# Kernel tuning notes

Hardware: AMD Instinct MI355X
Metric: run time of the kernel (lower is better)

The kernel has to match this reference:

```python
import jax, jax.numpy as jnp
import numpy as np

EMBED_DIM = 1024
NUM_HEADS = 16
HEAD_DIM = EMBED_DIM // NUM_HEADS
SEQ_LEN = 2048
BATCH = 2
THETA_BASE = 10000.0


def rope_angles(head_dim, max_seq_len):
    inv_freq = 1.0 / (THETA_BASE ** (jnp.arange(0, head_dim, 2, dtype=jnp.float32) / head_dim))
    pos = jnp.arange(max_seq_len, dtype=jnp.float32)
    angles = pos[:, None] * inv_freq[None, :]              # [S, D/2]
    angles = jnp.concatenate([angles, angles], axis=-1)    # [S, D]
    return jnp.cos(angles), jnp.sin(angles)


def apply_rope(x, cos, sin):
    # x: [B, H, S, D]; cos/sin: [S, D]
    d = x.shape[-1]
    x1, x2 = x[..., : d // 2], x[..., d // 2 :]
    rotated = jnp.concatenate([-x2, x1], axis=-1)
    return x * cos[None, None, :, :] + rotated * sin[None, None, :, :]


def setup_inputs() -> dict:
    key = jax.random.key(0)
    kx, kq, kk, kv, ko = jax.random.split(key, 5)
    s = 1.0 / np.sqrt(EMBED_DIM)
    return {
        "x": jax.random.normal(kx, (BATCH, SEQ_LEN, EMBED_DIM), dtype=jnp.float32),
        "Wq": jax.random.normal(kq, (EMBED_DIM, EMBED_DIM), dtype=jnp.float32) * s,
        "Wk": jax.random.normal(kk, (EMBED_DIM, EMBED_DIM), dtype=jnp.float32) * s,
        "Wv": jax.random.normal(kv, (EMBED_DIM, EMBED_DIM), dtype=jnp.float32) * s,
        "Wo": jax.random.normal(ko, (EMBED_DIM, EMBED_DIM), dtype=jnp.float32) * s,
    }


def reference(x, Wq, Wk, Wv, Wo):
    B, S, E = x.shape
    H, D = NUM_HEADS, HEAD_DIM
    cos, sin = rope_angles(D, S)

    def split_heads(t):
        return t.reshape(B, S, H, D).transpose(0, 2, 1, 3)  # [B,H,S,D]

    q = split_heads(x @ Wq.T)
    k = split_heads(x @ Wk.T)
    v = split_heads(x @ Wv.T)

    q = apply_rope(q, cos, sin)
    k = apply_rope(k, cos, sin)

    scores = jnp.einsum("bhsd,bhtd->bhst", q, k)
    causal = jnp.triu(jnp.ones((S, S), dtype=bool), k=1)
    scores = jnp.where(causal[None, None, :, :], -jnp.inf, scores)
    weights = jax.nn.softmax(scores / jnp.sqrt(jnp.float32(D)), axis=-1)

    ctx = jnp.einsum("bhst,bhtd->bhsd", weights, v)
    ctx = ctx.transpose(0, 2, 1, 3).reshape(B, S, E)
    return ctx @ Wo.T
```

## Files before the change

### kernel.cpp

```cpp
#include <hip/hip_runtime.h>
#include <hip/hip_bf16.h>

#define H_NUM 16
#define D_DIM 64
#define S_LEN 2048
#define EMB   1024
#define M_TOT 4096

typedef unsigned short u16;
typedef unsigned int   u32;
typedef __attribute__((ext_vector_type(8))) short short8;
typedef __attribute__((ext_vector_type(4))) float f32x4;

__device__ __forceinline__ u32 f2bf_u(float f) {
    u32 u = __float_as_uint(f);
    return (u + 0x7fffu + ((u >> 16) & 1u)) >> 16;
}
__device__ __forceinline__ u32 pack2(float a, float b) {
    return f2bf_u(a) | (f2bf_u(b) << 16);
}
__device__ __forceinline__ u32 pack2t(float a, float b) {
    return __builtin_amdgcn_perm(__float_as_uint(b), __float_as_uint(a),
                                 0x07060302u);
}
__device__ __forceinline__ uint4 pack8(float4 lo, float4 hi) {
    return make_uint4(pack2(lo.x, lo.y), pack2(lo.z, lo.w),
                      pack2(hi.x, hi.y), pack2(hi.z, hi.w));
}

__device__ __forceinline__ void lds_dma16(const u16* g, u16* l) {
    __builtin_amdgcn_global_load_lds(
        (const __attribute__((address_space(1))) void*)g,
        (__attribute__((address_space(3))) void*)l, 16, 0, 0);
}

__global__ __launch_bounds__(256) void cast_kernel(
    const float* __restrict__ x,  const float* __restrict__ Wq,
    const float* __restrict__ Wk, const float* __restrict__ Wv,
    const float* __restrict__ Wo, u16* __restrict__ ws, float2* __restrict__ tab)
{
    const int seg = blockIdx.y;
    if (seg == 5) {
        const int idx = blockIdx.x * 256 + threadIdx.x;
        if (idx < S_LEN * 32) {
            const int s = idx >> 5, d = idx & 31;
            const float ang = (float)s * __expf(-(float)d * 0.28782313662425573f);
            tab[idx] = make_float2(cosf(ang), sinf(ang));
        }
        return;
    }
    const float* src = (seg == 0) ? x : (seg == 1) ? Wq : (seg == 2) ? Wk
                     : (seg == 3) ? Wv : Wo;
    u16* dst = (seg == 0) ? ws : ws + (3 + seg) * 1048576;
    const int n = (seg == 0) ? 4194304 : 1048576;
    const int idx = (blockIdx.x * 256 + threadIdx.x) * 8;
    if (idx < n) {
        float4 lo = *(const float4*)(src + idx);
        float4 hi = *(const float4*)(src + idx + 4);
        *(uint4*)(dst + idx) = pack8(lo, hi);
    }
}

__global__ __launch_bounds__(256) void qkv_rope_kernel(
    const u16* __restrict__ xb, const u16* __restrict__ wb,
    const float2* __restrict__ tab,
    u16* __restrict__ qo, u16* __restrict__ ko, u16* __restrict__ vo)
{
    const int w  = blockIdx.y >> 3;
    const int nb = blockIdx.y & 7;
    const u16* W = wb + w * 1048576;

    __shared__ __align__(16) u16 smem[12288];
    u16* As = smem;
    u16* Bs = smem + 64 * 64;
    u16 (*Ep)[132] = (u16(*)[132])smem;

    const int tid   = threadIdx.x;
    const int lane  = tid & 63;
    const int wid   = tid >> 6;
    const int waveM = wid >> 1;
    const int waveN = wid & 1;
    const int col16 = lane & 15;
    const int quad  = lane >> 4;

    const int m0 = blockIdx.x * 64;
    const int n0 = nb * 128;

    f32x4 acc[2][4];
    const f32x4 zero4 = {0.f, 0.f, 0.f, 0.f};
#pragma unroll
    for (int i = 0; i < 2; i++)
#pragma unroll
        for (int j = 0; j < 4; j++) acc[i][j] = zero4;

    const int drow = tid >> 3;
    const int dpos = tid & 7;
    const u16* Ag = xb + (size_t)m0 * EMB;
    const u16* Bg = W  + (size_t)n0 * EMB;

    for (int k0 = 0; k0 < EMB; k0 += 64) {
        __syncthreads();
#pragma unroll
        for (int j = 0; j < 2; j++) {
            const int rl = j * 32 + drow;
            const int cg = dpos ^ (rl & 7);
            lds_dma16(Ag + (size_t)rl * EMB + k0 + cg * 8,
                      As + (j * 32 + wid * 8) * 64);
        }
#pragma unroll
        for (int j = 0; j < 4; j++) {
            const int rl = j * 32 + drow;
            const int cg = dpos ^ (rl & 7);
            lds_dma16(Bg + (size_t)rl * EMB + k0 + cg * 8,
                      Bs + (j * 32 + wid * 8) * 64);
        }
        __syncthreads();

        short8 af[2][2], bf[4][2];
#pragma unroll
        for (int mt = 0; mt < 2; mt++) {
            const int r = waveM * 32 + mt * 16 + col16;
#pragma unroll
            for (int ks = 0; ks < 2; ks++) {
                const int p = (ks * 4 + quad) ^ (r & 7);
                af[mt][ks] = *(const short8*)(As + r * 64 + p * 8);
            }
        }
#pragma unroll
        for (int nt = 0; nt < 4; nt++) {
            const int r = waveN * 64 + nt * 16 + col16;
#pragma unroll
            for (int ks = 0; ks < 2; ks++) {
                const int p = (ks * 4 + quad) ^ (r & 7);
                bf[nt][ks] = *(const short8*)(Bs + r * 64 + p * 8);
            }
        }
#pragma unroll
        for (int ks = 0; ks < 2; ks++)
#pragma unroll
            for (int mt = 0; mt < 2; mt++)
#pragma unroll
                for (int nt = 0; nt < 4; nt++)
                    acc[mt][nt] = __builtin_amdgcn_mfma_f32_16x16x32_bf16(
                        af[mt][ks], bf[nt][ks], acc[mt][nt], 0, 0, 0);
    }

    const float qs = (w == 0) ? 0.18033688011112042f : 1.0f;
    __syncthreads();
#pragma unroll
    for (int mt = 0; mt < 2; mt++) {
#pragma unroll
        for (int r = 0; r < 4; r++) {
            const int m_local = waveM * 32 + mt * 16 + quad * 4 + r;
            const int s = (m0 + m_local) & 2047;
            if (w == 2) {
#pragma unroll
                for (int nt = 0; nt < 4; nt++)
                    Ep[m_local][waveN * 64 + nt * 16 + col16] =
                        (u16)f2bf_u(acc[mt][nt][r]);
            } else {
#pragma unroll
                for (int nt = 0; nt < 2; nt++) {
                    const int d = nt * 16 + col16;
                    const float2 cs = tab[s * 32 + d];
                    const float lo = acc[mt][nt][r];
                    const float hi = acc[mt][nt + 2][r];
                    Ep[m_local][waveN * 64 + d]      =
                        (u16)f2bf_u((lo * cs.x - hi * cs.y) * qs);
                    Ep[m_local][waveN * 64 + d + 32] =
                        (u16)f2bf_u((hi * cs.x + lo * cs.y) * qs);
                }
            }
        }
    }
    __syncthreads();

    const int b = m0 >> 11;
    if (w != 2) {
        u16* out = (w == 0) ? qo : ko;
#pragma unroll
        for (int j = 0; j < 4; j++) {
            const int g = j * 256 + tid;
            const int head_local = g >> 9;
            const int sl  = (g >> 3) & 63;
            const int cir = g & 7;
            uint4 val = *(const uint4*)(&Ep[sl][head_local * 64 + cir * 8]);
            const int h = (n0 >> 6) + head_local;
            const size_t base = (((size_t)(b * H_NUM + h)) * S_LEN + (m0 & 2047)) * 64;
            *(uint4*)(out + base + (size_t)(g & 511) * 8) = val;
        }
    } else {
        const int s0 = m0 & 2047;
#pragma unroll
        for (int j = 0; j < 4; j++) {
            const int g = j * 256 + tid;
            const int d_all = g >> 3;
            const int sc = g & 7;
            u32 wv[4];
#pragma unroll
            for (int hw = 0; hw < 4; hw++) {
                const int p0 = sc * 8 + hw * 2;
                const int r0 = ((p0 & 3) << 4) | (p0 >> 2);
                const int p1 = p0 + 1;
                const int r1 = ((p1 & 3) << 4) | (p1 >> 2);
                wv[hw] = (u32)Ep[r0][d_all] | ((u32)Ep[r1][d_all] << 16);
            }
            const int h = (n0 >> 6) + (d_all >> 6);
            const int d = d_all & 63;
            *(uint4*)(vo + ((size_t)(b * H_NUM + h) * 64 + d) * 2048 + s0 + sc * 8) =
                make_uint4(wv[0], wv[1], wv[2], wv[3]);
        }
    }
}

__global__ __launch_bounds__(256) void attn_kernel(
    const u16* __restrict__ q, const u16* __restrict__ k,
    const u16* __restrict__ v, u16* __restrict__ ctx)
{
    __shared__ __align__(16) u16 QPA[64 * 64];
    __shared__ __align__(16) u16 QPB[64 * 64];
    __shared__ __align__(16) u16 Ks[2][64 * 64];
    __shared__ __align__(16) u16 VTs[2][64 * 64];

    const int tid   = threadIdx.x;
    const int lane  = tid & 63;
    const int wid   = tid >> 6;
    const int col16 = lane & 15;
    const int quad  = lane >> 4;

    const int bh = blockIdx.x;
    const int p  = blockIdx.y;
    const int qbA = p;
    const int qbB = 31 - p;
    const int qBaseA = qbA * 64;
    const int qBaseB = qbB * 64;
    const size_t bhOff = (size_t)bh * S_LEN * D_DIM;

    const int drow = tid >> 3;
    const int dpos = tid & 7;

    auto stage = [&](int kt, int buf) {
#pragma unroll
        for (int j = 0; j < 2; j++) {
            const int rl = j * 32 + drow;
            const int cg = dpos ^ (rl & 7);
            lds_dma16(k + bhOff + (size_t)(kt * 64 + rl) * 64 + cg * 8,
                      &Ks[buf][(j * 32 + wid * 8) * 64]);
        }
#pragma unroll
        for (int j = 0; j < 2; j++) {
            const int rl = j * 32 + drow;
            const int cg = dpos ^ (rl & 7);
            lds_dma16(v + bhOff + (size_t)rl * 2048 + kt * 64 + cg * 8,
                      &VTs[buf][(j * 32 + wid * 8) * 64]);
        }
    };

    stage(0, 0);
#pragma unroll
    for (int j = 0; j < 2; j++) {
        const int rl = j * 32 + drow;
        const int cg = dpos ^ (rl & 7);
        lds_dma16(q + bhOff + (size_t)(qBaseA + rl) * 64 + cg * 8,
                  QPA + (j * 32 + wid * 8) * 64);
        lds_dma16(q + bhOff + (size_t)(qBaseB + rl) * 64 + cg * 8,
                  QPB + (j * 32 + wid * 8) * 64);
    }
    __syncthreads();

    short8 qfA[2], qfB[2];
    {
        const int rq = wid * 16 + col16;
#pragma unroll
        for (int ks = 0; ks < 2; ks++) {
            const int c = (ks * 4 + quad) ^ (rq & 7);
            qfA[ks] = *(const short8*)(QPA + rq * 64 + c * 8);
            qfB[ks] = *(const short8*)(QPB + rq * 64 + c * 8);
        }
    }

    const short ONE = (short)0x3F80;
    const short8 onesf = {ONE, ONE, ONE, ONE, ONE, ONE, ONE, ONE};

    f32x4 OA[4], OB[4];
    const f32x4 zero4 = {0.f, 0.f, 0.f, 0.f};
#pragma unroll
    for (int j = 0; j < 4; j++) { OA[j] = zero4; OB[j] = zero4; }
    f32x4 laccA = zero4, laccB = zero4;

    auto process = [&](const short8* qf, u16* QP, f32x4* O, f32x4& lacc,
                       int qBase, bool diag, int kt, int cur) {
        f32x4 sc[4];
#pragma unroll
        for (int nt = 0; nt < 4; nt++) sc[nt] = zero4;
#pragma unroll
        for (int ks = 0; ks < 2; ks++) {
            short8 kf[4];
#pragma unroll
            for (int nt = 0; nt < 4; nt++) {
                const int rk = nt * 16 + col16;
                const int c = (ks * 4 + quad) ^ (rk & 7);
                kf[nt] = *(const short8*)(&Ks[cur][rk * 64 + c * 8]);
            }
            __builtin_amdgcn_s_setprio(1);
#pragma unroll
            for (int nt = 0; nt < 4; nt++)
                sc[nt] = __builtin_amdgcn_mfma_f32_16x16x32_bf16(
                    qf[ks], kf[nt], sc[nt], 0, 0, 0);
            __builtin_amdgcn_s_setprio(0);
        }

        if (diag) {
#pragma unroll
            for (int r = 0; r < 4; r++) {
                const int qg = qBase + wid * 16 + quad * 4 + r;
#pragma unroll
                for (int nt = 0; nt < 4; nt++) {
                    const int kg = kt * 64 + nt * 16 + col16;
                    float pv = __builtin_amdgcn_exp2f(sc[nt][r]);
                    if (kg > qg) pv = 0.f;
                    sc[nt][r] = pv;
                }
            }
        } else {
#pragma unroll
            for (int r = 0; r < 4; r++) {
#pragma unroll
                for (int nt = 0; nt < 4; nt++)
                    sc[nt][r] = __builtin_amdgcn_exp2f(sc[nt][r]);
            }
        }

#pragma unroll
        for (int r = 0; r < 4; r++) {
            const int ml = quad * 4 + r;
            const u32 lo = pack2t(sc[0][r], sc[1][r]);
            const u32 hi = pack2t(sc[2][r], sc[3][r]);
            *(uint2*)(QP + (wid * 16 + ml) * 64 +
                      (((col16 >> 1) ^ (ml & 7)) * 8 + (col16 & 1) * 4)) =
                make_uint2(lo, hi);
        }

#pragma unroll
        for (int ks = 0; ks < 2; ks++) {
            short8 pf, vf[4];
            {
                const int c = (ks * 4 + quad) ^ (col16 & 7);
                pf = *(const short8*)(QP + (wid * 16 + col16) * 64 + c * 8);
            }
#pragma unroll
            for (int dt = 0; dt < 4; dt++) {
                const int d = dt * 16 + col16;
                const int c = (ks * 4 + quad) ^ (d & 7);
                vf[dt] = *(const short8*)(&VTs[cur][d * 64 + c * 8]);
            }
            __builtin_amdgcn_s_setprio(1);
#pragma unroll
            for (int dt = 0; dt < 4; dt++)
                O[dt] = __builtin_amdgcn_mfma_f32_16x16x32_bf16(
                    pf, vf[dt], O[dt], 0, 0, 0);
            lacc = __builtin_amdgcn_mfma_f32_16x16x32_bf16(
                pf, onesf, lacc, 0, 0, 0);
            __builtin_amdgcn_s_setprio(0);
        }
    };

    for (int kt = 0; kt <= qbB; kt++) {
        if (kt > 0) __syncthreads();
        if (kt < qbB) stage(kt + 1, (kt + 1) & 1);
        const int cur = kt & 1;

        process(qfB, QPB, OB, laccB, qBaseB, kt == qbB, kt, cur);
        if (kt <= qbA)
            process(qfA, QPA, OA, laccA, qBaseA, kt == qbA, kt, cur);
    }

    const int b = bh >> 4, h = bh & 15;
    auto epilogue = [&](u16* QP, f32x4* O, f32x4& lacc, int qBase) {
#pragma unroll
        for (int r = 0; r < 4; r++) {
            const int ml = quad * 4 + r;
            const float inv = __builtin_amdgcn_rcpf(lacc[r]);
            const u32 lo = pack2t(O[0][r] * inv, O[1][r] * inv);
            const u32 hi = pack2t(O[2][r] * inv, O[3][r] * inv);
            *(uint2*)(QP + (wid * 16 + ml) * 64 +
                      (((col16 >> 1) ^ (ml & 7)) * 8 + (col16 & 1) * 4)) =
                make_uint2(lo, hi);
        }
#pragma unroll
        for (int j = 0; j < 2; j++) {
            const int gg  = j * 64 + lane;
            const int sl = gg >> 3;
            const int cir = gg & 7;
            u32 wv[4];
#pragma unroll
            for (int hw = 0; hw < 4; hw++) {
                const int d0 = cir * 8 + hw * 2;
                const int p0 = ((d0 & 15) << 2) | (d0 >> 4);
                const int d1 = d0 + 1;
                const int p1 = ((d1 & 15) << 2) | (d1 >> 4);
                const u16 v0 = QP[(wid * 16 + sl) * 64 + ((p0 >> 3) ^ (sl & 7)) * 8 + (p0 & 7)];
                const u16 v1 = QP[(wid * 16 + sl) * 64 + ((p1 >> 3) ^ (sl & 7)) * 8 + (p1 & 7)];
                wv[hw] = (u32)v0 | ((u32)v1 << 16);
            }
            const size_t rowbase =
                ((size_t)b * S_LEN + qBase + wid * 16 + sl) * EMB + h * 64;
            *(uint4*)(ctx + rowbase + cir * 8) = make_uint4(wv[0], wv[1], wv[2], wv[3]);
        }
    };
    epilogue(QPA, OA, laccA, qBaseA);
    epilogue(QPB, OB, laccB, qBaseB);
}

__global__ __launch_bounds__(256) void proj_kernel(
    const u16* __restrict__ X, const u16* __restrict__ W, float* __restrict__ out)
{
    __shared__ __align__(16) u16 smem[8192];
    u16* As = smem;
    u16* Bs = smem + 64 * 64;

    const int tid   = threadIdx.x;
    const int lane  = tid & 63;
    const int wid   = tid >> 6;
    const int col16 = lane & 15;
    const int quad  = lane >> 4;

    const int m0 = blockIdx.x * 64;
    const int n0 = blockIdx.y * 64;

    f32x4 acc[4];
    const f32x4 zero4 = {0.f, 0.f, 0.f, 0.f};
#pragma unroll
    for (int i = 0; i < 4; i++) acc[i] = zero4;

    const int drow = tid >> 3;
    const int dpos = tid & 7;
    const u16* Ag = X + (size_t)m0 * EMB;
    const u16* Bg = W + (size_t)n0 * EMB;

    for (int k0 = 0; k0 < EMB; k0 += 64) {
        __syncthreads();
#pragma unroll
        for (int j = 0; j < 2; j++) {
            const int rl = j * 32 + drow;
            const int cg = dpos ^ (rl & 7);
            lds_dma16(Ag + (size_t)rl * EMB + k0 + cg * 8,
                      As + (j * 32 + wid * 8) * 64);
        }
#pragma unroll
        for (int j = 0; j < 2; j++) {
            const int rl = j * 32 + drow;
            const int cg = dpos ^ (rl & 7);
            lds_dma16(Bg + (size_t)rl * EMB + k0 + cg * 8,
                      Bs + (j * 32 + wid * 8) * 64);
        }
        __syncthreads();

        short8 af[2], bf[4][2];
        {
            const int r = wid * 16 + col16;
#pragma unroll
            for (int ks = 0; ks < 2; ks++) {
                const int p = (ks * 4 + quad) ^ (r & 7);
                af[ks] = *(const short8*)(As + r * 64 + p * 8);
            }
        }
#pragma unroll
        for (int nt = 0; nt < 4; nt++) {
            const int r = nt * 16 + col16;
#pragma unroll
            for (int ks = 0; ks < 2; ks++) {
                const int p = (ks * 4 + quad) ^ (r & 7);
                bf[nt][ks] = *(const short8*)(Bs + r * 64 + p * 8);
            }
        }
#pragma unroll
        for (int ks = 0; ks < 2; ks++)
#pragma unroll
            for (int nt = 0; nt < 4; nt++)
                acc[nt] = __builtin_amdgcn_mfma_f32_16x16x32_bf16(
                    bf[nt][ks], af[ks], acc[nt], 0, 0, 0);
    }

#pragma unroll
    for (int nt = 0; nt < 4; nt++) {
        const int m_g = m0 + wid * 16 + col16;
        const int n_g = n0 + nt * 16 + quad * 4;
        *(f32x4*)(out + (size_t)m_g * EMB + n_g) = acc[nt];
    }
}

extern "C" void kernel_launch(void* const* d_in, const int* in_sizes, int n_in,
                              void* d_out, int out_size, void* d_ws, size_t ws_size,
                              hipStream_t stream)
{
    const float* x  = (const float*)d_in[0];
    const float* Wq = (const float*)d_in[1];
    const float* Wk = (const float*)d_in[2];
    const float* Wv = (const float*)d_in[3];
    const float* Wo = (const float*)d_in[4];

    u16* ws = (u16*)d_ws;
    u16* xb  = ws;
    u16* wb  = ws + 4194304;
    u16* wob = ws + 7340032;
    u16* q   = ws + 8388608;
    u16* k   = ws + 12582912;
    u16* v   = ws + 16777216;
    u16* ctx = ws + 20971520;
    float2* tab = (float2*)(ws + 25165824);

    cast_kernel<<<dim3(2048, 6), 256, 0, stream>>>(x, Wq, Wk, Wv, Wo, ws, tab);
    qkv_rope_kernel<<<dim3(64, 24), 256, 0, stream>>>(xb, wb, tab, q, k, v);
    attn_kernel<<<dim3(32, 16), 256, 0, stream>>>(q, k, v, ctx);
    proj_kernel<<<dim3(64, 16), 256, 0, stream>>>(ctx, wob, (float*)d_out);
}
```

Before: 166.3 us.

## Enlarge QKV GEMM tile to 128 rows and interleave attention's two query blocks

The QKV+RoPE GEMM now computes a 128x128 tile per block, with each wave holding 4x4 accumulators. Its epilogue is split into two passes through the shared staging buffer, and the grid is halved. This raises operand reuse per LDS load at the cost of more registers and fewer blocks. The attention kernel fuses the two query-block passes into one loop body, so the K and V fragments loaded from LDS are shared between both blocks and the MFMAs can interleave, which also increases register pressure.

```diff
diff --git a/kernel.cpp b/kernel.cpp
--- a/kernel.cpp
+++ b/kernel.cpp
@@ -70,9 +70,9 @@
     const int nb = blockIdx.y & 7;
     const u16* W = wb + w * 1048576;
 
-    __shared__ __align__(16) u16 smem[12288];
+    __shared__ __align__(16) u16 smem[16384];
     u16* As = smem;
-    u16* Bs = smem + 64 * 64;
+    u16* Bs = smem + 128 * 64;
     u16 (*Ep)[132] = (u16(*)[132])smem;
 
     const int tid   = threadIdx.x;
@@ -83,13 +83,13 @@
     const int col16 = lane & 15;
     const int quad  = lane >> 4;
 
-    const int m0 = blockIdx.x * 64;
+    const int m0 = blockIdx.x * 128;
     const int n0 = nb * 128;
 
-    f32x4 acc[2][4];
+    f32x4 acc[4][4];
     const f32x4 zero4 = {0.f, 0.f, 0.f, 0.f};
 #pragma unroll
-    for (int i = 0; i < 2; i++)
+    for (int i = 0; i < 4; i++)
 #pragma unroll
         for (int j = 0; j < 4; j++) acc[i][j] = zero4;
 
@@ -101,7 +101,7 @@
     for (int k0 = 0; k0 < EMB; k0 += 64) {
         __syncthreads();
 #pragma unroll
-        for (int j = 0; j < 2; j++) {
+        for (int j = 0; j < 4; j++) {
             const int rl = j * 32 + drow;
             const int cg = dpos ^ (rl & 7);
             lds_dma16(Ag + (size_t)rl * EMB + k0 + cg * 8,
@@ -116,99 +116,103 @@
         }
         __syncthreads();
 
-        short8 af[2][2], bf[4][2];
-#pragma unroll
-        for (int mt = 0; mt < 2; mt++) {
-            const int r = waveM * 32 + mt * 16 + col16;
-#pragma unroll
-            for (int ks = 0; ks < 2; ks++) {
+#pragma unroll
+        for (int ks = 0; ks < 2; ks++) {
+            short8 af[4], bf[4];
+#pragma unroll
+            for (int mt = 0; mt < 4; mt++) {
+                const int r = waveM * 64 + mt * 16 + col16;
                 const int p = (ks * 4 + quad) ^ (r & 7);
-                af[mt][ks] = *(const short8*)(As + r * 64 + p * 8);
-            }
-        }
-#pragma unroll
-        for (int nt = 0; nt < 4; nt++) {
-            const int r = waveN * 64 + nt * 16 + col16;
-#pragma unroll
-            for (int ks = 0; ks < 2; ks++) {
+                af[mt] = *(const short8*)(As + r * 64 + p * 8);
+            }
+#pragma unroll
+            for (int nt = 0; nt < 4; nt++) {
+                const int r = waveN * 64 + nt * 16 + col16;
                 const int p = (ks * 4 + quad) ^ (r & 7);
-                bf[nt][ks] = *(const short8*)(Bs + r * 64 + p * 8);
-            }
-        }
-#pragma unroll
-        for (int ks = 0; ks < 2; ks++)
-#pragma unroll
-            for (int mt = 0; mt < 2; mt++)
+                bf[nt] = *(const short8*)(Bs + r * 64 + p * 8);
+            }
+            __builtin_amdgcn_s_setprio(1);
+#pragma unroll
+            for (int mt = 0; mt < 4; mt++)
 #pragma unroll
                 for (int nt = 0; nt < 4; nt++)
                     acc[mt][nt] = __builtin_amdgcn_mfma_f32_16x16x32_bf16(
-                        af[mt][ks], bf[nt][ks], acc[mt][nt], 0, 0, 0);
+                        af[mt], bf[nt], acc[mt][nt], 0, 0, 0);
+            __builtin_amdgcn_s_setprio(0);
+        }
     }
 
     const float qs = (w == 0) ? 0.18033688011112042f : 1.0f;
-    __syncthreads();
-#pragma unroll
-    for (int mt = 0; mt < 2; mt++) {
-#pragma unroll
-        for (int r = 0; r < 4; r++) {
-            const int m_local = waveM * 32 + mt * 16 + quad * 4 + r;
-            const int s = (m0 + m_local) & 2047;
-            if (w == 2) {
-#pragma unroll
-                for (int nt = 0; nt < 4; nt++)
-                    Ep[m_local][waveN * 64 + nt * 16 + col16] =
-                        (u16)f2bf_u(acc[mt][nt][r]);
-            } else {
-#pragma unroll
-                for (int nt = 0; nt < 2; nt++) {
-                    const int d = nt * 16 + col16;
-                    const float2 cs = tab[s * 32 + d];
-                    const float lo = acc[mt][nt][r];
-                    const float hi = acc[mt][nt + 2][r];
-                    Ep[m_local][waveN * 64 + d]      =
-                        (u16)f2bf_u((lo * cs.x - hi * cs.y) * qs);
-                    Ep[m_local][waveN * 64 + d + 32] =
-                        (u16)f2bf_u((hi * cs.x + lo * cs.y) * qs);
+    const int b = m0 >> 11;
+#pragma unroll
+    for (int pass = 0; pass < 2; pass++) {
+        __syncthreads();
+        if (waveM == pass) {
+#pragma unroll
+            for (int mt = 0; mt < 4; mt++) {
+#pragma unroll
+                for (int r = 0; r < 4; r++) {
+                    const int m_local = mt * 16 + quad * 4 + r;
+                    const int s = (m0 + pass * 64 + m_local) & 2047;
+                    if (w == 2) {
+#pragma unroll
+                        for (int nt = 0; nt < 4; nt++)
+                            Ep[m_local][waveN * 64 + nt * 16 + col16] =
+                                (u16)f2bf_u(acc[mt][nt][r]);
+                    } else {
+#pragma unroll
+                        for (int nt = 0; nt < 2; nt++) {
+                            const int d = nt * 16 + col16;
+                            const float2 cs = tab[s * 32 + d];
+                            const float lo = acc[mt][nt][r];
+                            const float hi = acc[mt][nt + 2][r];
+                            Ep[m_local][waveN * 64 + d]      =
+                                (u16)f2bf_u((lo * cs.x - hi * cs.y) * qs);
+                            Ep[m_local][waveN * 64 + d + 32] =
+                                (u16)f2bf_u((hi * cs.x + lo * cs.y) * qs);
+                        }
+                    }
                 }
             }
         }
-    }
-    __syncthreads();
-
-    const int b = m0 >> 11;
-    if (w != 2) {
-        u16* out = (w == 0) ? qo : ko;
-#pragma unroll
-        for (int j = 0; j < 4; j++) {
-            const int g = j * 256 + tid;
-            const int head_local = g >> 9;
-            const int sl  = (g >> 3) & 63;
-            const int cir = g & 7;
-            uint4 val = *(const uint4*)(&Ep[sl][head_local * 64 + cir * 8]);
-            const int h = (n0 >> 6) + head_local;
-            const size_t base = (((size_t)(b * H_NUM + h)) * S_LEN + (m0 & 2047)) * 64;
-            *(uint4*)(out + base + (size_t)(g & 511) * 8) = val;
-        }
-    } else {
-        const int s0 = m0 & 2047;
-#pragma unroll
-        for (int j = 0; j < 4; j++) {
-            const int g = j * 256 + tid;
-            const int d_all = g >> 3;
-            const int sc = g & 7;
-            u32 wv[4];
-#pragma unroll
-            for (int hw = 0; hw < 4; hw++) {
-                const int p0 = sc * 8 + hw * 2;
-                const int r0 = ((p0 & 3) << 4) | (p0 >> 2);
-                const int p1 = p0 + 1;
-                const int r1 = ((p1 & 3) << 4) | (p1 >> 2);
-                wv[hw] = (u32)Ep[r0][d_all] | ((u32)Ep[r1][d_all] << 16);
-            }
-            const int h = (n0 >> 6) + (d_all >> 6);
-            const int d = d_all & 63;
-            *(uint4*)(vo + ((size_t)(b * H_NUM + h) * 64 + d) * 2048 + s0 + sc * 8) =
-                make_uint4(wv[0], wv[1], wv[2], wv[3]);
+        __syncthreads();
+
+        if (w != 2) {
+            u16* out = (w == 0) ? qo : ko;
+            const int sBase = (m0 + pass * 64) & 2047;
+#pragma unroll
+            for (int j = 0; j < 4; j++) {
+                const int g = j * 256 + tid;
+                const int head_local = g >> 9;
+                const int sl  = (g >> 3) & 63;
+                const int cir = g & 7;
+                uint4 val = *(const uint4*)(&Ep[sl][head_local * 64 + cir * 8]);
+                const int h = (n0 >> 6) + head_local;
+                const size_t base =
+                    (((size_t)(b * H_NUM + h)) * S_LEN + sBase) * 64;
+                *(uint4*)(out + base + (size_t)(g & 511) * 8) = val;
+            }
+        } else {
+            const int s0 = (m0 & 2047) + pass * 64;
+#pragma unroll
+            for (int j = 0; j < 4; j++) {
+                const int g = j * 256 + tid;
+                const int d_all = g >> 3;
+                const int sc = g & 7;
+                u32 wv[4];
+#pragma unroll
+                for (int hw = 0; hw < 4; hw++) {
+                    const int p0 = sc * 8 + hw * 2;
+                    const int r0 = ((p0 & 3) << 4) | (p0 >> 2);
+                    const int p1 = p0 + 1;
+                    const int r1 = ((p1 & 3) << 4) | (p1 >> 2);
+                    wv[hw] = (u32)Ep[r0][d_all] | ((u32)Ep[r1][d_all] << 16);
+                }
+                const int h = (n0 >> 6) + (d_all >> 6);
+                const int d = d_all & 63;
+                *(uint4*)(vo + ((size_t)(b * H_NUM + h) * 64 + d) * 2048 +
+                          s0 + sc * 8) = make_uint4(wv[0], wv[1], wv[2], wv[3]);
+            }
         }
     }
 }
@@ -288,11 +292,17 @@
     for (int j = 0; j < 4; j++) { OA[j] = zero4; OB[j] = zero4; }
     f32x4 laccA = zero4, laccB = zero4;
 
-    auto process = [&](const short8* qf, u16* QP, f32x4* O, f32x4& lacc,
-                       int qBase, bool diag, int kt, int cur) {
-        f32x4 sc[4];
-#pragma unroll
-        for (int nt = 0; nt < 4; nt++) sc[nt] = zero4;
+    const int qgRow = wid * 16 + quad * 4;
+
+    for (int kt = 0; kt <= qbB; kt++) {
+        if (kt > 0) __syncthreads();
+        if (kt < qbB) stage(kt + 1, (kt + 1) & 1);
+        const int cur = kt & 1;
+        const bool doA = (kt <= qbA);
+
+        f32x4 scB[4], scA[4];
+#pragma unroll
+        for (int nt = 0; nt < 4; nt++) { scB[nt] = zero4; scA[nt] = zero4; }
 #pragma unroll
         for (int ks = 0; ks < 2; ks++) {
             short8 kf[4];
@@ -305,74 +315,104 @@
             __builtin_amdgcn_s_setprio(1);
 #pragma unroll
             for (int nt = 0; nt < 4; nt++)
-                sc[nt] = __builtin_amdgcn_mfma_f32_16x16x32_bf16(
-                    qf[ks], kf[nt], sc[nt], 0, 0, 0);
+                scB[nt] = __builtin_amdgcn_mfma_f32_16x16x32_bf16(
+                    qfB[ks], kf[nt], scB[nt], 0, 0, 0);
+            if (doA) {
+#pragma unroll
+                for (int nt = 0; nt < 4; nt++)
+                    scA[nt] = __builtin_amdgcn_mfma_f32_16x16x32_bf16(
+                        qfA[ks], kf[nt], scA[nt], 0, 0, 0);
+            }
             __builtin_amdgcn_s_setprio(0);
         }
 
-        if (diag) {
+        if (kt == qbB) {
 #pragma unroll
             for (int r = 0; r < 4; r++) {
-                const int qg = qBase + wid * 16 + quad * 4 + r;
+                const int qg = qBaseB + qgRow + r;
 #pragma unroll
                 for (int nt = 0; nt < 4; nt++) {
                     const int kg = kt * 64 + nt * 16 + col16;
-                    float pv = __builtin_amdgcn_exp2f(sc[nt][r]);
+                    float pv = __builtin_amdgcn_exp2f(scB[nt][r]);
                     if (kg > qg) pv = 0.f;
-                    sc[nt][r] = pv;
+                    scB[nt][r] = pv;
                 }
             }
         } else {
 #pragma unroll
-            for (int r = 0; r < 4; r++) {
+            for (int r = 0; r < 4; r++)
 #pragma unroll
                 for (int nt = 0; nt < 4; nt++)
-                    sc[nt][r] = __builtin_amdgcn_exp2f(sc[nt][r]);
+                    scB[nt][r] = __builtin_amdgcn_exp2f(scB[nt][r]);
+        }
+        if (doA) {
+            if (kt == qbA) {
+#pragma unroll
+                for (int r = 0; r < 4; r++) {
+                    const int qg = qBaseA + qgRow + r;
+#pragma unroll
+                    for (int nt = 0; nt < 4; nt++) {
+                        const int kg = kt * 64 + nt * 16 + col16;
+                        float pv = __builtin_amdgcn_exp2f(scA[nt][r]);
+                        if (kg > qg) pv = 0.f;
+                        scA[nt][r] = pv;
+                    }
+                }
+            } else {
+#pragma unroll
+                for (int r = 0; r < 4; r++)
+#pragma unroll
+                    for (int nt = 0; nt < 4; nt++)
+                        scA[nt][r] = __builtin_amdgcn_exp2f(scA[nt][r]);
             }
         }
 
 #pragma unroll
         for (int r = 0; r < 4; r++) {
             const int ml = quad * 4 + r;
-            const u32 lo = pack2t(sc[0][r], sc[1][r]);
-            const u32 hi = pack2t(sc[2][r], sc[3][r]);
-            *(uint2*)(QP + (wid * 16 + ml) * 64 +
-                      (((col16 >> 1) ^ (ml & 7)) * 8 + (col16 & 1) * 4)) =
-                make_uint2(lo, hi);
+            const int off = (wid * 16 + ml) * 64 +
+                            (((col16 >> 1) ^ (ml & 7)) * 8 + (col16 & 1) * 4);
+            *(uint2*)(QPB + off) =
+                make_uint2(pack2t(scB[0][r], scB[1][r]),
+                           pack2t(scB[2][r], scB[3][r]));
+            if (doA)
+                *(uint2*)(QPA + off) =
+                    make_uint2(pack2t(scA[0][r], scA[1][r]),
+                               pack2t(scA[2][r], scA[3][r]));
         }
 
 #pragma unroll
         for (int ks = 0; ks < 2; ks++) {
-            short8 pf, vf[4];
-            {
-                const int c = (ks * 4 + quad) ^ (col16 & 7);
-                pf = *(const short8*)(QP + (wid * 16 + col16) * 64 + c * 8);
-            }
+            short8 vf[4];
 #pragma unroll
             for (int dt = 0; dt < 4; dt++) {
                 const int d = dt * 16 + col16;
                 const int c = (ks * 4 + quad) ^ (d & 7);
                 vf[dt] = *(const short8*)(&VTs[cur][d * 64 + c * 8]);
             }
+            const int cpf = (ks * 4 + quad) ^ (col16 & 7);
+            const int pfOff = (wid * 16 + col16) * 64 + cpf * 8;
+            short8 pfB = *(const short8*)(QPB + pfOff);
             __builtin_amdgcn_s_setprio(1);
 #pragma unroll
             for (int dt = 0; dt < 4; dt++)
-                O[dt] = __builtin_amdgcn_mfma_f32_16x16x32_bf16(
-                    pf, vf[dt], O[dt], 0, 0, 0);
-            lacc = __builtin_amdgcn_mfma_f32_16x16x32_bf16(
-                pf, onesf, lacc, 0, 0, 0);
+                OB[dt] = __builtin_amdgcn_mfma_f32_16x16x32_bf16(
+                    pfB, vf[dt], OB[dt], 0, 0, 0);
+            laccB = __builtin_amdgcn_mfma_f32_16x16x32_bf16(
+                pfB, onesf, laccB, 0, 0, 0);
             __builtin_amdgcn_s_setprio(0);
-        }
-    };
-
-    for (int kt = 0; kt <= qbB; kt++) {
-        if (kt > 0) __syncthreads();
-        if (kt < qbB) stage(kt + 1, (kt + 1) & 1);
-        const int cur = kt & 1;
-
-        process(qfB, QPB, OB, laccB, qBaseB, kt == qbB, kt, cur);
-        if (kt <= qbA)
-            process(qfA, QPA, OA, laccA, qBaseA, kt == qbA, kt, cur);
+            if (doA) {
+                short8 pfA = *(const short8*)(QPA + pfOff);
+                __builtin_amdgcn_s_setprio(1);
+#pragma unroll
+                for (int dt = 0; dt < 4; dt++)
+                    OA[dt] = __builtin_amdgcn_mfma_f32_16x16x32_bf16(
+                        pfA, vf[dt], OA[dt], 0, 0, 0);
+                laccA = __builtin_amdgcn_mfma_f32_16x16x32_bf16(
+                    pfA, onesf, laccA, 0, 0, 0);
+                __builtin_amdgcn_s_setprio(0);
+            }
+        }
     }
 
     const int b = bh >> 4, h = bh & 15;
@@ -511,7 +551,7 @@
     float2* tab = (float2*)(ws + 25165824);
 
     cast_kernel<<<dim3(2048, 6), 256, 0, stream>>>(x, Wq, Wk, Wv, Wo, ws, tab);
-    qkv_rope_kernel<<<dim3(64, 24), 256, 0, stream>>>(xb, wb, tab, q, k, v);
+    qkv_rope_kernel<<<dim3(32, 24), 256, 0, stream>>>(xb, wb, tab, q, k, v);
     attn_kernel<<<dim3(32, 16), 256, 0, stream>>>(q, k, v, ctx);
     proj_kernel<<<dim3(64, 16), 256, 0, stream>>>(ctx, wob, (float*)d_out);
 }
```

After: 190.3 us. 1.14x slower.

## Split paired query tiles across two wave groups in 512-thread attention blocks

Applied to the files above, without the earlier changes.

The attention kernel now launches 512 threads per block. Waves 0-3 handle the short query tile A and waves 4-7 handle the long tile B, where before each wave processed both tiles one after the other. K/V staging is spread across all 8 waves, one DMA each per tile. The aim is more waves in flight per CU and shorter serial MFMA chains per wave. In exchange, the A waves sit idle at barriers once their tile finishes, which leaves the work imbalanced, and larger blocks may lower occupancy.

```diff
diff --git a/kernel.cpp b/kernel.cpp
--- a/kernel.cpp
+++ b/kernel.cpp
@@ -213,7 +213,7 @@
     }
 }
 
-__global__ __launch_bounds__(256) void attn_kernel(
+__global__ __launch_bounds__(512) void attn_kernel(
     const u16* __restrict__ q, const u16* __restrict__ k,
     const u16* __restrict__ v, u16* __restrict__ ctx)
 {
@@ -225,6 +225,8 @@
     const int tid   = threadIdx.x;
     const int lane  = tid & 63;
     const int wid   = tid >> 6;
+    const int w4    = wid & 3;
+    const bool isB  = (wid >= 4);
     const int col16 = lane & 15;
     const int quad  = lane >> 4;
 
@@ -232,64 +234,62 @@
     const int p  = blockIdx.y;
     const int qbA = p;
     const int qbB = 31 - p;
-    const int qBaseA = qbA * 64;
-    const int qBaseB = qbB * 64;
+    const int myQb   = isB ? qbB : qbA;
+    const int myBase = myQb * 64;
     const size_t bhOff = (size_t)bh * S_LEN * D_DIM;
 
-    const int drow = tid >> 3;
-    const int dpos = tid & 7;
+    const int srow = tid >> 3;
+    const int spos = tid & 7;
+    const int scg  = spos ^ (srow & 7);
+
+    u16* qdst = isB ? QPB : QPA;
 
     auto stage = [&](int kt, int buf) {
+        lds_dma16(k + bhOff + (size_t)(kt * 64 + srow) * 64 + scg * 8,
+                  &Ks[buf][wid * 512]);
+        lds_dma16(v + bhOff + (size_t)srow * 2048 + kt * 64 + scg * 8,
+                  &VTs[buf][wid * 512]);
+    };
+
+    stage(0, 0);
+    {
+        const int r5 = srow & 31;
 #pragma unroll
         for (int j = 0; j < 2; j++) {
-            const int rl = j * 32 + drow;
-            const int cg = dpos ^ (rl & 7);
-            lds_dma16(k + bhOff + (size_t)(kt * 64 + rl) * 64 + cg * 8,
-                      &Ks[buf][(j * 32 + wid * 8) * 64]);
-        }
-#pragma unroll
-        for (int j = 0; j < 2; j++) {
-            const int rl = j * 32 + drow;
-            const int cg = dpos ^ (rl & 7);
-            lds_dma16(v + bhOff + (size_t)rl * 2048 + kt * 64 + cg * 8,
-                      &VTs[buf][(j * 32 + wid * 8) * 64]);
-        }
-    };
-
-    stage(0, 0);
-#pragma unroll
-    for (int j = 0; j < 2; j++) {
-        const int rl = j * 32 + drow;
-        const int cg = dpos ^ (rl & 7);
-        lds_dma16(q + bhOff + (size_t)(qBaseA + rl) * 64 + cg * 8,
-                  QPA + (j * 32 + wid * 8) * 64);
-        lds_dma16(q + bhOff + (size_t)(qBaseB + rl) * 64 + cg * 8,
-                  QPB + (j * 32 + wid * 8) * 64);
+            const int rl = j * 32 + r5;
+            const int cg = spos ^ (rl & 7);
+            lds_dma16(q + bhOff + (size_t)(myBase + rl) * 64 + cg * 8,
+                      qdst + (j * 32 + w4 * 8) * 64);
+        }
     }
     __syncthreads();
 
-    short8 qfA[2], qfB[2];
+    short8 qf[2];
     {
-        const int rq = wid * 16 + col16;
+        const int rq = w4 * 16 + col16;
 #pragma unroll
         for (int ks = 0; ks < 2; ks++) {
             const int c = (ks * 4 + quad) ^ (rq & 7);
-            qfA[ks] = *(const short8*)(QPA + rq * 64 + c * 8);
-            qfB[ks] = *(const short8*)(QPB + rq * 64 + c * 8);
+            qf[ks] = *(const short8*)(qdst + rq * 64 + c * 8);
         }
     }
 
     const short ONE = (short)0x3F80;
     const short8 onesf = {ONE, ONE, ONE, ONE, ONE, ONE, ONE, ONE};
 
-    f32x4 OA[4], OB[4];
+    f32x4 O[4];
     const f32x4 zero4 = {0.f, 0.f, 0.f, 0.f};
 #pragma unroll
-    for (int j = 0; j < 4; j++) { OA[j] = zero4; OB[j] = zero4; }
-    f32x4 laccA = zero4, laccB = zero4;
-
-    auto process = [&](const short8* qf, u16* QP, f32x4* O, f32x4& lacc,
-                       int qBase, bool diag, int kt, int cur) {
+    for (int j = 0; j < 4; j++) O[j] = zero4;
+    f32x4 lacc = zero4;
+
+    for (int kt = 0; kt <= qbB; kt++) {
+        if (kt > 0) __syncthreads();
+        if (kt < qbB) stage(kt + 1, (kt + 1) & 1);
+        const int cur = kt & 1;
+
+        if (kt > myQb) continue;
+
         f32x4 sc[4];
 #pragma unroll
         for (int nt = 0; nt < 4; nt++) sc[nt] = zero4;
@@ -310,10 +310,10 @@
             __builtin_amdgcn_s_setprio(0);
         }
 
-        if (diag) {
+        if (kt == myQb) {
 #pragma unroll
             for (int r = 0; r < 4; r++) {
-                const int qg = qBase + wid * 16 + quad * 4 + r;
+                const int qg = myBase + w4 * 16 + quad * 4 + r;
 #pragma unroll
                 for (int nt = 0; nt < 4; nt++) {
                     const int kg = kt * 64 + nt * 16 + col16;
@@ -324,11 +324,10 @@
             }
         } else {
 #pragma unroll
-            for (int r = 0; r < 4; r++) {
+            for (int r = 0; r < 4; r++)
 #pragma unroll
                 for (int nt = 0; nt < 4; nt++)
                     sc[nt][r] = __builtin_amdgcn_exp2f(sc[nt][r]);
-            }
         }
 
 #pragma unroll
@@ -336,7 +335,7 @@
             const int ml = quad * 4 + r;
             const u32 lo = pack2t(sc[0][r], sc[1][r]);
             const u32 hi = pack2t(sc[2][r], sc[3][r]);
-            *(uint2*)(QP + (wid * 16 + ml) * 64 +
+            *(uint2*)(qdst + (w4 * 16 + ml) * 64 +
                       (((col16 >> 1) ^ (ml & 7)) * 8 + (col16 & 1) * 4)) =
                 make_uint2(lo, hi);
         }
@@ -346,7 +345,7 @@
             short8 pf, vf[4];
             {
                 const int c = (ks * 4 + quad) ^ (col16 & 7);
-                pf = *(const short8*)(QP + (wid * 16 + col16) * 64 + c * 8);
+                pf = *(const short8*)(qdst + (w4 * 16 + col16) * 64 + c * 8);
             }
 #pragma unroll
             for (int dt = 0; dt < 4; dt++) {
@@ -363,53 +362,39 @@
                 pf, onesf, lacc, 0, 0, 0);
             __builtin_amdgcn_s_setprio(0);
         }
-    };
-
-    for (int kt = 0; kt <= qbB; kt++) {
-        if (kt > 0) __syncthreads();
-        if (kt < qbB) stage(kt + 1, (kt + 1) & 1);
-        const int cur = kt & 1;
-
-        process(qfB, QPB, OB, laccB, qBaseB, kt == qbB, kt, cur);
-        if (kt <= qbA)
-            process(qfA, QPA, OA, laccA, qBaseA, kt == qbA, kt, cur);
     }
 
     const int b = bh >> 4, h = bh & 15;
-    auto epilogue = [&](u16* QP, f32x4* O, f32x4& lacc, int qBase) {
-#pragma unroll
-        for (int r = 0; r < 4; r++) {
-            const int ml = quad * 4 + r;
-            const float inv = __builtin_amdgcn_rcpf(lacc[r]);
-            const u32 lo = pack2t(O[0][r] * inv, O[1][r] * inv);
-            const u32 hi = pack2t(O[2][r] * inv, O[3][r] * inv);
-            *(uint2*)(QP + (wid * 16 + ml) * 64 +
-                      (((col16 >> 1) ^ (ml & 7)) * 8 + (col16 & 1) * 4)) =
-                make_uint2(lo, hi);
-        }
-#pragma unroll
-        for (int j = 0; j < 2; j++) {
-            const int gg  = j * 64 + lane;
-            const int sl = gg >> 3;
-            const int cir = gg & 7;
-            u32 wv[4];
-#pragma unroll
-            for (int hw = 0; hw < 4; hw++) {
-                const int d0 = cir * 8 + hw * 2;
-                const int p0 = ((d0 & 15) << 2) | (d0 >> 4);
-                const int d1 = d0 + 1;
-                const int p1 = ((d1 & 15) << 2) | (d1 >> 4);
-                const u16 v0 = QP[(wid * 16 + sl) * 64 + ((p0 >> 3) ^ (sl & 7)) * 8 + (p0 & 7)];
-                const u16 v1 = QP[(wid * 16 + sl) * 64 + ((p1 >> 3) ^ (sl & 7)) * 8 + (p1 & 7)];
-                wv[hw] = (u32)v0 | ((u32)v1 << 16);
-            }
-            const size_t rowbase =
-                ((size_t)b * S_LEN + qBase + wid * 16 + sl) * EMB + h * 64;
-            *(uint4*)(ctx + rowbase + cir * 8) = make_uint4(wv[0], wv[1], wv[2], wv[3]);
-        }
-    };
-    epilogue(QPA, OA, laccA, qBaseA);
-    epilogue(QPB, OB, laccB, qBaseB);
+#pragma unroll
+    for (int r = 0; r < 4; r++) {
+        const int ml = quad * 4 + r;
+        const float inv = __builtin_amdgcn_rcpf(lacc[r]);
+        const u32 lo = pack2t(O[0][r] * inv, O[1][r] * inv);
+        const u32 hi = pack2t(O[2][r] * inv, O[3][r] * inv);
+        *(uint2*)(qdst + (w4 * 16 + ml) * 64 +
+                  (((col16 >> 1) ^ (ml & 7)) * 8 + (col16 & 1) * 4)) =
+            make_uint2(lo, hi);
+    }
+#pragma unroll
+    for (int j = 0; j < 2; j++) {
+        const int gg  = j * 64 + lane;
+        const int sl = gg >> 3;
+        const int cir = gg & 7;
+        u32 wv[4];
+#pragma unroll
+        for (int hw = 0; hw < 4; hw++) {
+            const int d0 = cir * 8 + hw * 2;
+            const int p0 = ((d0 & 15) << 2) | (d0 >> 4);
+            const int d1 = d0 + 1;
+            const int p1 = ((d1 & 15) << 2) | (d1 >> 4);
+            const u16 v0 = qdst[(w4 * 16 + sl) * 64 + ((p0 >> 3) ^ (sl & 7)) * 8 + (p0 & 7)];
+            const u16 v1 = qdst[(w4 * 16 + sl) * 64 + ((p1 >> 3) ^ (sl & 7)) * 8 + (p1 & 7)];
+            wv[hw] = (u32)v0 | ((u32)v1 << 16);
+        }
+        const size_t rowbase =
+            ((size_t)b * S_LEN + myBase + w4 * 16 + sl) * EMB + h * 64;
+        *(uint4*)(ctx + rowbase + cir * 8) = make_uint4(wv[0], wv[1], wv[2], wv[3]);
+    }
 }
 
 __global__ __launch_bounds__(256) void proj_kernel(
@@ -512,6 +497,6 @@
 
     cast_kernel<<<dim3(2048, 6), 256, 0, stream>>>(x, Wq, Wk, Wv, Wo, ws, tab);
     qkv_rope_kernel<<<dim3(64, 24), 256, 0, stream>>>(xb, wb, tab, q, k, v);
-    attn_kernel<<<dim3(32, 16), 256, 0, stream>>>(q, k, v, ctx);
+    attn_kernel<<<dim3(32, 16), 512, 0, stream>>>(q, k, v, ctx);
     proj_kernel<<<dim3(64, 16), 256, 0, stream>>>(ctx, wob, (float*)d_out);
 }
```

Result: no change. 164.3 us (-1.2%).
